# Kernel tuning notes

Hardware: AMD Instinct MI355X
Metric: run time of the kernel (lower is better)

The kernel has to match this reference:

```python
import jax, jax.numpy as jnp
import numpy as np
import math

S = 64.0
M = 0.5
COS_M = math.cos(M)
SIN_M = math.sin(M)
TH = math.cos(math.pi - M)
MM = math.sin(math.pi - M) * M
NUM_CLASSES = 100000
EMB_DIM = 512
BATCH = 512
EPS_CLAMP = 1e-07


def setup_inputs() -> dict:
    key = jax.random.key(0)
    k1, k2, k3 = jax.random.split(key, 3)
    embeddings = jax.random.normal(k1, (BATCH, EMB_DIM), dtype=jnp.float32)
    weight = jax.random.normal(k2, (NUM_CLASSES, EMB_DIM), dtype=jnp.float32)
    labels = jax.random.randint(k3, (BATCH,), 0, NUM_CLASSES, dtype=jnp.int64)
    return {"embeddings": embeddings, "weight": weight, "labels": labels}


def _l2_normalize(x, axis=-1, eps=1e-12):
    # matches F.normalize(p=2): divide by max(norm, eps)
    norm = jnp.sqrt(jnp.sum(x * x, axis=axis, keepdims=True))
    return x / jnp.maximum(norm, eps)


def reference(embeddings, weight, labels):
    e = _l2_normalize(embeddings, axis=1)          # [B, D]
    w = _l2_normalize(weight, axis=1)              # [C, D]
    cosine = jnp.clip(e @ w.T, -1.0 + EPS_CLAMP, 1.0 - EPS_CLAMP)  # [B, C]
    sine = jnp.sqrt(1.0 - cosine * cosine)
    phi = cosine * COS_M - sine * SIN_M
    phi = jnp.where(cosine > TH, phi, cosine - MM)
    one_hot = jax.nn.one_hot(labels, NUM_CLASSES, dtype=cosine.dtype)
    logits = (one_hot * phi + (1.0 - one_hot) * cosine) * S
    # cross-entropy with mean reduction
    logp = jax.nn.log_softmax(logits, axis=-1)
    nll = -jnp.take_along_axis(logp, labels[:, None], axis=1)[:, 0]
    return jnp.mean(nll)
```

## Files before the change

### kernel.cpp

```cpp
#include <hip/hip_runtime.h>
#include <math.h>

#define BATCH 512
#define DIM 512
#define NCLS 100000
#define NB_TILES 391
#define NPART 1564
#define NB_TILES_FB 782
#define S_SCALE 64.0f
#define COS_M 0.8775825618903728f
#define SIN_M 0.479425538604203f
#define TH_C (-0.8775825618903728f)
#define MM_C 0.2397127693021015f
#define CLIP_LO (-1.0f + 1e-7f)
#define CLIP_HI (1.0f - 1e-7f)

typedef __attribute__((ext_vector_type(8))) short bf16x8;
typedef __attribute__((ext_vector_type(4))) float f32x4;

__device__ __forceinline__ unsigned int f2bf(float x) {
    union { float f; unsigned int u; } v;
    v.f = x;
    return (v.u + 0x7fffu + ((v.u >> 16) & 1u)) >> 16;
}
__device__ __forceinline__ unsigned int pack2(float lo, float hi) {
    return f2bf(lo) | (f2bf(hi) << 16);
}

__device__ __forceinline__ void gld_lds16(const void* g, void* l) {
    __builtin_amdgcn_global_load_lds(
        (const __attribute__((address_space(1))) void*)g,
        (__attribute__((address_space(3))) void*)l, 16, 0, 0);
}

__global__ void k_norm_e(const float* __restrict__ e, short* __restrict__ ebf,
                         float* __restrict__ sumexpz) {
    int row = blockIdx.x;
    int tid = threadIdx.x;
    const float4* p = (const float4*)(e + (size_t)row * DIM);
    float4 v = p[tid];
    float ss = v.x * v.x + v.y * v.y + v.z * v.z + v.w * v.w;
    for (int m = 1; m < 64; m <<= 1) ss += __shfl_xor(ss, m, 64);
    __shared__ float wss[2];
    if ((tid & 63) == 0) wss[tid >> 6] = ss;
    __syncthreads();
    float inv = 1.0f / fmaxf(sqrtf(wss[0] + wss[1]), 1e-12f);
    ushort4 o;
    o.x = (unsigned short)f2bf(v.x * inv);
    o.y = (unsigned short)f2bf(v.y * inv);
    o.z = (unsigned short)f2bf(v.z * inv);
    o.w = (unsigned short)f2bf(v.w * inv);
    ((ushort4*)(ebf + (size_t)row * DIM))[tid] = o;
    if (tid == 0) sumexpz[row] = 0.0f;
}

__global__ void k_wconv(const float* __restrict__ w, short* __restrict__ wbf,
                        float* __restrict__ wnorm) {
    int tid = threadIdx.x;
    int wv = tid >> 6, lane = tid & 63;
    int row = blockIdx.x * 4 + wv;
    const float4* src = (const float4*)(w + (size_t)row * DIM);
    float4 a = src[lane];
    float4 b = src[64 + lane];
    float ssq = a.x * a.x + a.y * a.y + a.z * a.z + a.w * a.w +
                b.x * b.x + b.y * b.y + b.z * b.z + b.w * b.w;
#pragma unroll
    for (int m = 1; m < 64; m <<= 1) ssq += __shfl_xor(ssq, m, 64);
    ushort4 oa, ob;
    oa.x = (unsigned short)f2bf(a.x);
    oa.y = (unsigned short)f2bf(a.y);
    oa.z = (unsigned short)f2bf(a.z);
    oa.w = (unsigned short)f2bf(a.w);
    ob.x = (unsigned short)f2bf(b.x);
    ob.y = (unsigned short)f2bf(b.y);
    ob.z = (unsigned short)f2bf(b.z);
    ob.w = (unsigned short)f2bf(b.w);
    ushort4* dst = (ushort4*)(wbf + (size_t)row * DIM);
    dst[lane] = oa;
    dst[64 + lane] = ob;
    if (lane == 0) wnorm[row] = 1.0f / fmaxf(sqrtf(ssq), 1e-12f);
}

__global__ __launch_bounds__(512, 4) void k_gemm2(
    const short* __restrict__ ebf, const short* __restrict__ wbf,
    const float* __restrict__ wnorm, const int* __restrict__ labels,
    float* __restrict__ partial, float* __restrict__ phiS) {
    __shared__ __align__(16) short As[3][4096];
    __shared__ __align__(16) short Bs[3][8192];
    __shared__ int sLbl[128];

    int bx = blockIdx.x;
    int nb = (bx >> 5) * 8 + (bx & 7);
    if (nb >= NB_TILES) return;
    int mb = (bx >> 3) & 3;
    int n0 = nb * 256;

    int tid = threadIdx.x;
    int lane = tid & 63;
    int wv = tid >> 6;
    int wm = wv >> 2, wn = wv & 3;
    int quad = lane >> 4, l16 = lane & 15;

    int g = (lane & 3) ^ (((lane >> 2) ^ (lane >> 4)) & 3);
    int r0 = wv * 16 + (lane >> 2);
    const char* gA = (const char*)ebf + (size_t)(mb * 128 + r0) * (DIM * 2) + g * 16;
    int wr0 = n0 + r0;       if (wr0 > NCLS - 1) wr0 = NCLS - 1;
    int wr1 = n0 + 128 + r0; if (wr1 > NCLS - 1) wr1 = NCLS - 1;
    const char* gB0 = (const char*)wbf + (size_t)wr0 * (DIM * 2) + g * 16;
    const char* gB1 = (const char*)wbf + (size_t)wr1 * (DIM * 2) + g * 16;
    int ldsw = wv * 1024;

#define STAGE(BUF, KC)                                                    \
    do {                                                                  \
        int kb_ = (KC) * 64;                                              \
        gld_lds16(gA + kb_, (char*)&As[BUF][0] + ldsw);                   \
        gld_lds16(gB0 + kb_, (char*)&Bs[BUF][0] + ldsw);                  \
        gld_lds16(gB1 + kb_, (char*)&Bs[BUF][0] + 8192 + ldsw);          \
    } while (0)

    STAGE(0, 0);
    STAGE(1, 1);

    if (tid < 128) sLbl[tid] = labels[mb * 128 + tid];

    f32x4 acc[4][4];
#pragma unroll
    for (int i = 0; i < 4; ++i)
#pragma unroll
        for (int j = 0; j < 4; ++j) acc[i][j] = (f32x4){0.f, 0.f, 0.f, 0.f};

    int go = (quad ^ ((l16 ^ (l16 >> 2)) & 3)) * 8;
    int arowb = (wm * 64 + l16) * 32 + go;
    int browb = (wn * 64 + l16) * 32 + go;

    asm volatile("s_waitcnt vmcnt(3)\n\ts_barrier" ::: "memory");

#pragma unroll
    for (int kc = 0; kc < 16; ++kc) {
        int cur = kc % 3;
        if (kc + 2 < 16) STAGE((kc + 2) % 3, kc + 2);
        {
            bf16x8 af[4], bfr[4];
#pragma unroll
            for (int t = 0; t < 4; ++t)
                af[t] = *(const bf16x8*)&As[cur][arowb + t * 16 * 32];
#pragma unroll
            for (int t = 0; t < 4; ++t)
                bfr[t] = *(const bf16x8*)&Bs[cur][browb + t * 16 * 32];
#pragma unroll
            for (int tm = 0; tm < 4; ++tm)
#pragma unroll
                for (int tn = 0; tn < 4; ++tn)
                    acc[tm][tn] = __builtin_amdgcn_mfma_f32_16x16x32_bf16(
                        af[tm], bfr[tn], acc[tm][tn], 0, 0, 0);
        }
        if (kc < 15) {
            if (kc + 2 < 16)
                asm volatile("s_waitcnt vmcnt(3)\n\ts_barrier" ::: "memory");
            else
                asm volatile("s_waitcnt vmcnt(0)\n\ts_barrier" ::: "memory");
        }
    }
#undef STAGE

    float wscale[4];
#pragma unroll
    for (int tn = 0; tn < 4; ++tn) {
        int col = n0 + wn * 64 + tn * 16 + l16;
        if (col > NCLS - 1) col = NCLS - 1;
        wscale[tn] = wnorm[col];
    }

    float rowsum[16];
#pragma unroll
    for (int i = 0; i < 16; ++i) rowsum[i] = 0.0f;

#pragma unroll
    for (int tm = 0; tm < 4; ++tm) {
#pragma unroll
        for (int r = 0; r < 4; ++r) {
            int m_local = wm * 64 + tm * 16 + quad * 4 + r;
            int lbl = sLbl[m_local];
            float rs = 0.0f;
#pragma unroll
            for (int tn = 0; tn < 4; ++tn) {
                float c = acc[tm][tn][r] * wscale[tn];
                c = fminf(fmaxf(c, CLIP_LO), CLIP_HI);
                int col = n0 + wn * 64 + tn * 16 + l16;
                float t = c;
                if (col == lbl) {
                    float sn = sqrtf(fmaxf(1.0f - c * c, 0.0f));
                    float ph = c * COS_M - sn * SIN_M;
                    ph = (c > TH_C) ? ph : (c - MM_C);
                    t = ph;
                    phiS[mb * 128 + m_local] = S_SCALE * ph;
                }
                float ex = (col < NCLS) ? __expf(S_SCALE * t - 64.0f) : 0.0f;
                rs += ex;
            }
            rowsum[tm * 4 + r] = rs;
        }
    }
    float* pbase = partial + (size_t)(nb * 4 + wn) * 512 + mb * 128;
#pragma unroll
    for (int idx = 0; idx < 16; ++idx) {
        float v = rowsum[idx];
        v += __shfl_xor(v, 1, 64);
        v += __shfl_xor(v, 2, 64);
        v += __shfl_xor(v, 4, 64);
        v += __shfl_xor(v, 8, 64);
        if (l16 == idx) {
            int tm = idx >> 2, r = idx & 3;
            int m_local = wm * 64 + tm * 16 + quad * 4 + r;
            pbase[m_local] = v;
        }
    }
}

__global__ void k_rownll(const float* __restrict__ partial,
                         float* __restrict__ part2) {
    int gid = blockIdx.x * 256 + threadIdx.x;
    int col = ((blockIdx.x & 1) << 8) | threadIdx.x;
    int seg = gid >> 9;
    int p0 = seg * 98;
    int p1 = p0 + 98; if (p1 > NPART) p1 = NPART;
    float s = 0.0f;
#pragma unroll 4
    for (int p = p0; p < p1; ++p) s += partial[(size_t)p * 512 + col];
    part2[seg * 512 + col] = s;
}

__global__ void k_final_mean(const float* __restrict__ part2,
                             const float* __restrict__ phiS,
                             float* __restrict__ out) {
    int tid = threadIdx.x;
    float s = 0.0f;
#pragma unroll
    for (int seg = 0; seg < 16; ++seg) s += part2[seg * 512 + tid];
    float nll = 64.0f + logf(s) - phiS[tid];
    for (int m = 1; m < 64; m <<= 1) nll += __shfl_xor(nll, m, 64);
    __shared__ float ws[8];
    if ((tid & 63) == 0) ws[tid >> 6] = nll;
    __syncthreads();
    if (tid == 0) {
        float t = 0.0f;
        for (int j = 0; j < 8; ++j) t += ws[j];
        out[0] = t / (float)BATCH;
    }
}

__global__ __launch_bounds__(256, 2) void k_gemm_fb(
    const short* __restrict__ ebf, const float* __restrict__ wgt,
    const int* __restrict__ labels, float* __restrict__ sumexp,
    float* __restrict__ phiS) {
    __shared__ __align__(16) short As[128 * 32];
    __shared__ __align__(16) short Bs[128 * 32];
    __shared__ int sLbl[128];
    __shared__ float sWn[128];

    int bx = blockIdx.x;
    int nb = (bx >> 5) * 8 + (bx & 7);
    if (nb >= NB_TILES_FB) return;
    int mb = (bx >> 3) & 3;
    int n0 = nb * 128;

    int tid = threadIdx.x;
    int lane = tid & 63;
    int wv = tid >> 6;
    int wm = wv >> 1, wn = wv & 1;
    int quad = lane >> 4, l16 = lane & 15;

    if (tid < 128) sLbl[tid] = labels[mb * 128 + tid];

    int ar = tid >> 2;
    const short* gA = ebf + (size_t)(mb * 128 + ar) * DIM + (tid & 3) * 8;
    int akey = ((tid >> 2) ^ (tid >> 4)) & 3;
    int aw0 = ar * 32 + ((tid & 3) ^ akey) * 8;

    int br = tid >> 3;
    int gBo[4];
#pragma unroll
    for (int i = 0; i < 4; ++i) {
        int wr = n0 + 32 * i + br;
        if (wr > NCLS - 1) wr = NCLS - 1;
        gBo[i] = wr * DIM + (tid & 7) * 4;
    }
    int bkey = ((tid >> 3) ^ (tid >> 5)) & 3;
    int bw0 = br * 32 + (((tid & 7) >> 1) ^ bkey) * 8 + (tid & 1) * 4;

    f32x4 acc[4][4];
#pragma unroll
    for (int i = 0; i < 4; ++i)
#pragma unroll
        for (int j = 0; j < 4; ++j) acc[i][j] = (f32x4){0.f, 0.f, 0.f, 0.f};
    float ssq[4] = {0.f, 0.f, 0.f, 0.f};

    int go = (quad ^ ((l16 ^ (l16 >> 2)) & 3)) * 8;
    int arowb = (wm * 64 + l16) * 32 + go;
    int browb = (wn * 64 + l16) * 32 + go;

    int4 ra0 = *(const int4*)(gA);
    int4 ra1 = *(const int4*)(gA + 64 * DIM);
    float4 rb0 = *(const float4*)(wgt + gBo[0]);
    float4 rb1 = *(const float4*)(wgt + gBo[1]);
    float4 rb2 = *(const float4*)(wgt + gBo[2]);
    float4 rb3 = *(const float4*)(wgt + gBo[3]);

#pragma unroll 1
    for (int kc = 0; kc < 16; ++kc) {
        *(int4*)&As[aw0] = ra0;
        *(int4*)&As[64 * 32 + aw0] = ra1;
        {
            uint2 p;
            ssq[0] += rb0.x * rb0.x + rb0.y * rb0.y + rb0.z * rb0.z + rb0.w * rb0.w;
            p.x = pack2(rb0.x, rb0.y); p.y = pack2(rb0.z, rb0.w);
            *(uint2*)&Bs[bw0] = p;
            ssq[1] += rb1.x * rb1.x + rb1.y * rb1.y + rb1.z * rb1.z + rb1.w * rb1.w;
            p.x = pack2(rb1.x, rb1.y); p.y = pack2(rb1.z, rb1.w);
            *(uint2*)&Bs[1024 + bw0] = p;
            ssq[2] += rb2.x * rb2.x + rb2.y * rb2.y + rb2.z * rb2.z + rb2.w * rb2.w;
            p.x = pack2(rb2.x, rb2.y); p.y = pack2(rb2.z, rb2.w);
            *(uint2*)&Bs[2048 + bw0] = p;
            ssq[3] += rb3.x * rb3.x + rb3.y * rb3.y + rb3.z * rb3.z + rb3.w * rb3.w;
            p.x = pack2(rb3.x, rb3.y); p.y = pack2(rb3.z, rb3.w);
            *(uint2*)&Bs[3072 + bw0] = p;
        }
        if (kc < 15) {
            int ko = (kc + 1) * 32;
            ra0 = *(const int4*)(gA + ko);
            ra1 = *(const int4*)(gA + 64 * DIM + ko);
            rb0 = *(const float4*)(wgt + gBo[0] + ko);
            rb1 = *(const float4*)(wgt + gBo[1] + ko);
            rb2 = *(const float4*)(wgt + gBo[2] + ko);
            rb3 = *(const float4*)(wgt + gBo[3] + ko);
        }
        asm volatile("s_waitcnt lgkmcnt(0)\n\ts_barrier" ::: "memory");
        {
            bf16x8 af[4], bfr[4];
#pragma unroll
            for (int t = 0; t < 4; ++t)
                af[t] = *(const bf16x8*)&As[arowb + t * 16 * 32];
#pragma unroll
            for (int t = 0; t < 4; ++t)
                bfr[t] = *(const bf16x8*)&Bs[browb + t * 16 * 32];
#pragma unroll
            for (int tm = 0; tm < 4; ++tm)
#pragma unroll
                for (int tn = 0; tn < 4; ++tn)
                    acc[tm][tn] = __builtin_amdgcn_mfma_f32_16x16x32_bf16(
                        af[tm], bfr[tn], acc[tm][tn], 0, 0, 0);
        }
        asm volatile("s_barrier" ::: "memory");
    }

#pragma unroll
    for (int i = 0; i < 4; ++i) {
        float s = ssq[i];
        s += __shfl_xor(s, 1, 64);
        s += __shfl_xor(s, 2, 64);
        s += __shfl_xor(s, 4, 64);
        if ((lane & 7) == 0)
            sWn[32 * i + br] = 1.0f / fmaxf(sqrtf(s), 1e-12f);
    }
    asm volatile("s_waitcnt lgkmcnt(0)\n\ts_barrier" ::: "memory");

    float wscale[4];
#pragma unroll
    for (int tn = 0; tn < 4; ++tn) wscale[tn] = sWn[wn * 64 + tn * 16 + l16];

    float rowsum[16];
#pragma unroll
    for (int i = 0; i < 16; ++i) rowsum[i] = 0.0f;

#pragma unroll
    for (int tm = 0; tm < 4; ++tm) {
#pragma unroll
        for (int r = 0; r < 4; ++r) {
            int m_local = wm * 64 + tm * 16 + quad * 4 + r;
            int lbl = sLbl[m_local];
            float rs = 0.0f;
#pragma unroll
            for (int tn = 0; tn < 4; ++tn) {
                float c = acc[tm][tn][r] * wscale[tn];
                c = fminf(fmaxf(c, CLIP_LO), CLIP_HI);
                int col = n0 + wn * 64 + tn * 16 + l16;
                float t = c;
                if (col == lbl) {
                    float sn = sqrtf(fmaxf(1.0f - c * c, 0.0f));
                    float ph = c * COS_M - sn * SIN_M;
                    ph = (c > TH_C) ? ph : (c - MM_C);
                    t = ph;
                    phiS[mb * 128 + m_local] = S_SCALE * ph;
                }
                float ex = (col < NCLS) ? __expf(S_SCALE * t - 64.0f) : 0.0f;
                rs += ex;
            }
            rowsum[tm * 4 + r] = rs;
        }
    }
#pragma unroll
    for (int idx = 0; idx < 16; ++idx) {
        float v = rowsum[idx];
        v += __shfl_xor(v, 1, 64);
        v += __shfl_xor(v, 2, 64);
        v += __shfl_xor(v, 4, 64);
        v += __shfl_xor(v, 8, 64);
        if (l16 == idx) {
            int tm = idx >> 2, r = idx & 3;
            int m_local = wm * 64 + tm * 16 + quad * 4 + r;
            atomicAdd(&sumexp[mb * 128 + m_local], v);
        }
    }
}

__global__ void k_final_fb(const float* __restrict__ sumexp,
                           const float* __restrict__ phiS,
                           float* __restrict__ out) {
    int tid = threadIdx.x;
    float nll = 64.0f + logf(sumexp[tid]) - phiS[tid];
    for (int m = 1; m < 64; m <<= 1) nll += __shfl_xor(nll, m, 64);
    __shared__ float ws[8];
    if ((tid & 63) == 0) ws[tid >> 6] = nll;
    __syncthreads();
    if (tid == 0) {
        float s = 0.0f;
        for (int j = 0; j < 8; ++j) s += ws[j];
        out[0] = s / (float)BATCH;
    }
}

extern "C" void kernel_launch(void* const* d_in, const int* in_sizes, int n_in,
                              void* d_out, int out_size, void* d_ws,
                              size_t ws_size, hipStream_t stream) {
    const float* emb = (const float*)d_in[0];
    const float* wgt = (const float*)d_in[1];
    const int* lbl = (const int*)d_in[2];

    char* ws = (char*)d_ws;
    short* ebf = (short*)ws;
    float* phiS = (float*)(ws + 524288);
    float* sumexp_fb = (float*)(ws + 526336);
    float* part2 = (float*)(ws + 528384);
    float* wnorm = (float*)(ws + 561152);
    float* partial = (float*)(ws + 1048576);
    short* wbf = (short*)(ws + 4251648);

    const size_t NEED = 4251648ull + 102400000ull;

    if (ws_size >= NEED) {
        k_wconv<<<dim3(NCLS / 4), dim3(256), 0, stream>>>(wgt, wbf, wnorm);
        k_norm_e<<<dim3(BATCH), dim3(128), 0, stream>>>(emb, ebf, sumexp_fb);
        k_gemm2<<<dim3(1568), dim3(512), 0, stream>>>(ebf, wbf, wnorm, lbl,
                                                      partial, phiS);
        k_rownll<<<dim3(32), dim3(256), 0, stream>>>(partial, part2);
        k_final_mean<<<dim3(1), dim3(512), 0, stream>>>(part2, phiS,
                                                        (float*)d_out);
    } else {
        k_norm_e<<<dim3(BATCH), dim3(128), 0, stream>>>(emb, ebf, sumexp_fb);
        k_gemm_fb<<<dim3(3136), dim3(256), 0, stream>>>(ebf, wgt, lbl,
                                                        sumexp_fb, phiS);
        k_final_fb<<<dim3(1), dim3(512), 0, stream>>>(sumexp_fb, phiS,
                                                      (float*)d_out);
    }
}
```

Baseline: 378.4 us.

## Use 4 waves per GEMM block with 64x128 warp tiles

Shrinks the GEMM block from 8 waves to 4 while keeping the 128x256 block tile. Each wave now computes a 64x128 tile with 32 MFMA accumulators and issues six global-to-LDS loads per stage. Partial sums per tile drop from 4 to 2 column groups, so the reduction and workspace layout are resized to match. The goal is more MFMA work per LDS fragment read and fewer partials, at the cost of roughly double the accumulator registers per wave, lower occupancy and fewer waves to hide memory latency.

Result: slower. 390.1 us (+3.1%).

```diff
diff --git a/kernel.cpp b/kernel.cpp
--- a/kernel.cpp
+++ b/kernel.cpp
@@ -5,7 +5,7 @@
 #define DIM 512
 #define NCLS 100000
 #define NB_TILES 391
-#define NPART 1564
+#define NPART 782
 #define NB_TILES_FB 782
 #define S_SCALE 64.0f
 #define COS_M 0.8775825618903728f
@@ -81,7 +81,7 @@
     if (lane == 0) wnorm[row] = 1.0f / fmaxf(sqrtf(ssq), 1e-12f);
 }
 
-__global__ __launch_bounds__(512, 4) void k_gemm2(
+__global__ __launch_bounds__(256, 2) void k_gemm2(
     const short* __restrict__ ebf, const short* __restrict__ wbf,
     const float* __restrict__ wnorm, const int* __restrict__ labels,
     float* __restrict__ partial, float* __restrict__ phiS) {
@@ -98,75 +98,91 @@
     int tid = threadIdx.x;
     int lane = tid & 63;
     int wv = tid >> 6;
-    int wm = wv >> 2, wn = wv & 3;
+    int wm = wv >> 1, wn = wv & 1;
     int quad = lane >> 4, l16 = lane & 15;
 
+    if (tid < 128) sLbl[tid] = labels[mb * 128 + tid];
+
     int g = (lane & 3) ^ (((lane >> 2) ^ (lane >> 4)) & 3);
-    int r0 = wv * 16 + (lane >> 2);
-    const char* gA = (const char*)ebf + (size_t)(mb * 128 + r0) * (DIM * 2) + g * 16;
-    int wr0 = n0 + r0;       if (wr0 > NCLS - 1) wr0 = NCLS - 1;
-    int wr1 = n0 + 128 + r0; if (wr1 > NCLS - 1) wr1 = NCLS - 1;
-    const char* gB0 = (const char*)wbf + (size_t)wr0 * (DIM * 2) + g * 16;
-    const char* gB1 = (const char*)wbf + (size_t)wr1 * (DIM * 2) + g * 16;
-    int ldsw = wv * 1024;
-
-#define STAGE(BUF, KC)                                                    \
-    do {                                                                  \
-        int kb_ = (KC) * 64;                                              \
-        gld_lds16(gA + kb_, (char*)&As[BUF][0] + ldsw);                   \
-        gld_lds16(gB0 + kb_, (char*)&Bs[BUF][0] + ldsw);                  \
-        gld_lds16(gB1 + kb_, (char*)&Bs[BUF][0] + 8192 + ldsw);          \
+    int rr = lane >> 2;
+    const char* gA0 =
+        (const char*)ebf + (size_t)(mb * 128 + wv * 32 + rr) * 1024 + g * 16;
+    const char* gA1 = gA0 + 16 * 1024;
+    const char* gB0;
+    const char* gB1;
+    const char* gB2;
+    const char* gB3;
+    {
+        int w0 = n0 + wv * 64 + rr;       if (w0 > NCLS - 1) w0 = NCLS - 1;
+        int w1 = n0 + wv * 64 + 16 + rr;  if (w1 > NCLS - 1) w1 = NCLS - 1;
+        int w2 = n0 + wv * 64 + 32 + rr;  if (w2 > NCLS - 1) w2 = NCLS - 1;
+        int w3 = n0 + wv * 64 + 48 + rr;  if (w3 > NCLS - 1) w3 = NCLS - 1;
+        gB0 = (const char*)wbf + (size_t)w0 * 1024 + g * 16;
+        gB1 = (const char*)wbf + (size_t)w1 * 1024 + g * 16;
+        gB2 = (const char*)wbf + (size_t)w2 * 1024 + g * 16;
+        gB3 = (const char*)wbf + (size_t)w3 * 1024 + g * 16;
+    }
+    int ldsA = wv * 2048;
+    int ldsB = wv * 4096;
+
+#define STAGE(BUF, KC)                                                   \
+    do {                                                                 \
+        int kb_ = (KC) * 64;                                             \
+        gld_lds16(gA0 + kb_, (char*)&As[BUF][0] + ldsA);                 \
+        gld_lds16(gA1 + kb_, (char*)&As[BUF][0] + ldsA + 1024);          \
+        gld_lds16(gB0 + kb_, (char*)&Bs[BUF][0] + ldsB);                 \
+        gld_lds16(gB1 + kb_, (char*)&Bs[BUF][0] + ldsB + 1024);         \
+        gld_lds16(gB2 + kb_, (char*)&Bs[BUF][0] + ldsB + 2048);         \
+        gld_lds16(gB3 + kb_, (char*)&Bs[BUF][0] + ldsB + 3072);         \
     } while (0)
 
     STAGE(0, 0);
     STAGE(1, 1);
 
-    if (tid < 128) sLbl[tid] = labels[mb * 128 + tid];
-
-    f32x4 acc[4][4];
+    f32x4 acc[4][8];
 #pragma unroll
     for (int i = 0; i < 4; ++i)
 #pragma unroll
-        for (int j = 0; j < 4; ++j) acc[i][j] = (f32x4){0.f, 0.f, 0.f, 0.f};
+        for (int j = 0; j < 8; ++j) acc[i][j] = (f32x4){0.f, 0.f, 0.f, 0.f};
 
     int go = (quad ^ ((l16 ^ (l16 >> 2)) & 3)) * 8;
     int arowb = (wm * 64 + l16) * 32 + go;
-    int browb = (wn * 64 + l16) * 32 + go;
-
-    asm volatile("s_waitcnt vmcnt(3)\n\ts_barrier" ::: "memory");
+    int browb = (wn * 128 + l16) * 32 + go;
+
+    asm volatile("s_waitcnt vmcnt(6)\n\ts_barrier" ::: "memory");
 
 #pragma unroll
     for (int kc = 0; kc < 16; ++kc) {
         int cur = kc % 3;
         if (kc + 2 < 16) STAGE((kc + 2) % 3, kc + 2);
         {
-            bf16x8 af[4], bfr[4];
+            bf16x8 af[4], bfr[8];
 #pragma unroll
             for (int t = 0; t < 4; ++t)
                 af[t] = *(const bf16x8*)&As[cur][arowb + t * 16 * 32];
 #pragma unroll
-            for (int t = 0; t < 4; ++t)
+            for (int t = 0; t < 8; ++t)
                 bfr[t] = *(const bf16x8*)&Bs[cur][browb + t * 16 * 32];
 #pragma unroll
             for (int tm = 0; tm < 4; ++tm)
 #pragma unroll
-                for (int tn = 0; tn < 4; ++tn)
+                for (int tn = 0; tn < 8; ++tn)
                     acc[tm][tn] = __builtin_amdgcn_mfma_f32_16x16x32_bf16(
                         af[tm], bfr[tn], acc[tm][tn], 0, 0, 0);
         }
         if (kc < 15) {
             if (kc + 2 < 16)
-                asm volatile("s_waitcnt vmcnt(3)\n\ts_barrier" ::: "memory");
+                asm volatile("s_waitcnt vmcnt(6)\n\ts_barrier" ::: "memory");
             else
                 asm volatile("s_waitcnt vmcnt(0)\n\ts_barrier" ::: "memory");
         }
     }
 #undef STAGE
 
-    float wscale[4];
-#pragma unroll
-    for (int tn = 0; tn < 4; ++tn) {
-        int col = n0 + wn * 64 + tn * 16 + l16;
+    float wscale[8];
+#pragma unroll
+    for (int tn = 0; tn < 8; ++tn) {
+        int col = n0 + wn * 128 + tn * 16 + l16;
         if (col > NCLS - 1) col = NCLS - 1;
         wscale[tn] = wnorm[col];
     }
@@ -183,10 +199,10 @@
             int lbl = sLbl[m_local];
             float rs = 0.0f;
 #pragma unroll
-            for (int tn = 0; tn < 4; ++tn) {
+            for (int tn = 0; tn < 8; ++tn) {
                 float c = acc[tm][tn][r] * wscale[tn];
                 c = fminf(fmaxf(c, CLIP_LO), CLIP_HI);
-                int col = n0 + wn * 64 + tn * 16 + l16;
+                int col = n0 + wn * 128 + tn * 16 + l16;
                 float t = c;
                 if (col == lbl) {
                     float sn = sqrtf(fmaxf(1.0f - c * c, 0.0f));
@@ -201,7 +217,7 @@
             rowsum[tm * 4 + r] = rs;
         }
     }
-    float* pbase = partial + (size_t)(nb * 4 + wn) * 512 + mb * 128;
+    float* pbase = partial + (size_t)(nb * 2 + wn) * 512 + mb * 128;
 #pragma unroll
     for (int idx = 0; idx < 16; ++idx) {
         float v = rowsum[idx];
@@ -222,8 +238,8 @@
     int gid = blockIdx.x * 256 + threadIdx.x;
     int col = ((blockIdx.x & 1) << 8) | threadIdx.x;
     int seg = gid >> 9;
-    int p0 = seg * 98;
-    int p1 = p0 + 98; if (p1 > NPART) p1 = NPART;
+    int p0 = seg * 49;
+    int p1 = p0 + 49; if (p1 > NPART) p1 = NPART;
     float s = 0.0f;
 #pragma unroll 4
     for (int p = p0; p < p1; ++p) s += partial[(size_t)p * 512 + col];
@@ -443,14 +459,14 @@
     float* part2 = (float*)(ws + 528384);
     float* wnorm = (float*)(ws + 561152);
     float* partial = (float*)(ws + 1048576);
-    short* wbf = (short*)(ws + 4251648);
-
-    const size_t NEED = 4251648ull + 102400000ull;
+    short* wbf = (short*)(ws + 2650112);
+
+    const size_t NEED = 2650112ull + 102400000ull;
 
     if (ws_size >= NEED) {
         k_wconv<<<dim3(NCLS / 4), dim3(256), 0, stream>>>(wgt, wbf, wnorm);
         k_norm_e<<<dim3(BATCH), dim3(128), 0, stream>>>(emb, ebf, sumexp_fb);
-        k_gemm2<<<dim3(1568), dim3(512), 0, stream>>>(ebf, wbf, wnorm, lbl,
+        k_gemm2<<<dim3(1568), dim3(256), 0, stream>>>(ebf, wbf, wnorm, lbl,
                                                       partial, phiS);
         k_rownll<<<dim3(32), dim3(256), 0, stream>>>(partial, part2);
         k_final_mean<<<dim3(1), dim3(512), 0, stream>>>(part2, phiS,
```

## Fuse weight bf16 conversion and norm computation into GEMM, retile to 256x128

Applied to the files above, without the earlier changes.

Removes the separate weight-conversion kernel that wrote a bf16 copy of the 100000x512 weight matrix plus per-row inverse norms. The GEMM now loads fp32 weights directly through registers, accumulates per-row sum of squares, packs to bf16 into LDS, and computes the inverse norms in shared memory. Tiles are reshaped so each block covers 256 batch rows by 128 classes, meaning each weight row is read once per block pair instead of four times. This avoids a full write and reread of the bf16 weight matrix, at the cost of register-staged B loads, lower occupancy, and twice the fp32 weight reads.

After: 404.4 us. 6.9% more time.

```diff
diff --git a/kernel.cpp b/kernel.cpp
--- a/kernel.cpp
+++ b/kernel.cpp
@@ -4,7 +4,7 @@
 #define BATCH 512
 #define DIM 512
 #define NCLS 100000
-#define NB_TILES 391
+#define NB_TILES 782
 #define NPART 1564
 #define NB_TILES_FB 782
 #define S_SCALE 64.0f
@@ -54,91 +54,98 @@
     if (tid == 0) sumexpz[row] = 0.0f;
 }
 
-__global__ void k_wconv(const float* __restrict__ w, short* __restrict__ wbf,
-                        float* __restrict__ wnorm) {
-    int tid = threadIdx.x;
-    int wv = tid >> 6, lane = tid & 63;
-    int row = blockIdx.x * 4 + wv;
-    const float4* src = (const float4*)(w + (size_t)row * DIM);
-    float4 a = src[lane];
-    float4 b = src[64 + lane];
-    float ssq = a.x * a.x + a.y * a.y + a.z * a.z + a.w * a.w +
-                b.x * b.x + b.y * b.y + b.z * b.z + b.w * b.w;
-#pragma unroll
-    for (int m = 1; m < 64; m <<= 1) ssq += __shfl_xor(ssq, m, 64);
-    ushort4 oa, ob;
-    oa.x = (unsigned short)f2bf(a.x);
-    oa.y = (unsigned short)f2bf(a.y);
-    oa.z = (unsigned short)f2bf(a.z);
-    oa.w = (unsigned short)f2bf(a.w);
-    ob.x = (unsigned short)f2bf(b.x);
-    ob.y = (unsigned short)f2bf(b.y);
-    ob.z = (unsigned short)f2bf(b.z);
-    ob.w = (unsigned short)f2bf(b.w);
-    ushort4* dst = (ushort4*)(wbf + (size_t)row * DIM);
-    dst[lane] = oa;
-    dst[64 + lane] = ob;
-    if (lane == 0) wnorm[row] = 1.0f / fmaxf(sqrtf(ssq), 1e-12f);
-}
-
-__global__ __launch_bounds__(512, 4) void k_gemm2(
-    const short* __restrict__ ebf, const short* __restrict__ wbf,
-    const float* __restrict__ wnorm, const int* __restrict__ labels,
-    float* __restrict__ partial, float* __restrict__ phiS) {
-    __shared__ __align__(16) short As[3][4096];
-    __shared__ __align__(16) short Bs[3][8192];
-    __shared__ int sLbl[128];
+__global__ __launch_bounds__(512, 2) void k_gemm3(
+    const short* __restrict__ ebf, const float* __restrict__ wgt,
+    const int* __restrict__ labels, float* __restrict__ partial,
+    float* __restrict__ phiS) {
+    __shared__ __align__(16) short As[3][8192];
+    __shared__ __align__(16) short Bs[3][4096];
+    __shared__ int sLbl[256];
+    __shared__ float sWn[128];
 
     int bx = blockIdx.x;
-    int nb = (bx >> 5) * 8 + (bx & 7);
+    int nb = (bx >> 4) * 8 + (bx & 7);
     if (nb >= NB_TILES) return;
-    int mb = (bx >> 3) & 3;
-    int n0 = nb * 256;
+    int mb = (bx >> 3) & 1;
+    int n0 = nb * 128;
 
     int tid = threadIdx.x;
     int lane = tid & 63;
     int wv = tid >> 6;
-    int wm = wv >> 2, wn = wv & 3;
+    int wm = wv >> 1, wn = wv & 1;
     int quad = lane >> 4, l16 = lane & 15;
 
+    if (tid < 256) sLbl[tid] = labels[mb * 256 + tid];
+
     int g = (lane & 3) ^ (((lane >> 2) ^ (lane >> 4)) & 3);
-    int r0 = wv * 16 + (lane >> 2);
-    const char* gA = (const char*)ebf + (size_t)(mb * 128 + r0) * (DIM * 2) + g * 16;
-    int wr0 = n0 + r0;       if (wr0 > NCLS - 1) wr0 = NCLS - 1;
-    int wr1 = n0 + 128 + r0; if (wr1 > NCLS - 1) wr1 = NCLS - 1;
-    const char* gB0 = (const char*)wbf + (size_t)wr0 * (DIM * 2) + g * 16;
-    const char* gB1 = (const char*)wbf + (size_t)wr1 * (DIM * 2) + g * 16;
-    int ldsw = wv * 1024;
-
-#define STAGE(BUF, KC)                                                    \
-    do {                                                                  \
-        int kb_ = (KC) * 64;                                              \
-        gld_lds16(gA + kb_, (char*)&As[BUF][0] + ldsw);                   \
-        gld_lds16(gB0 + kb_, (char*)&Bs[BUF][0] + ldsw);                  \
-        gld_lds16(gB1 + kb_, (char*)&Bs[BUF][0] + 8192 + ldsw);          \
+    const char* gA0 = (const char*)ebf +
+                      (size_t)(mb * 256 + wv * 32 + (lane >> 2)) * 1024 + g * 16;
+    const char* gA1 = gA0 + 16 * 1024;
+    int ldsA = wv * 2048;
+
+    int brow = tid >> 2;
+    int wr = n0 + brow;
+    if (wr > NCLS - 1) wr = NCLS - 1;
+    const float* gB = wgt + (size_t)wr * DIM + (tid & 3) * 8;
+    int bkey = (brow ^ (brow >> 2)) & 3;
+    int bw0 = brow * 32 + ((tid & 3) ^ bkey) * 8;
+
+#define STAGE_A(BUF, KC)                                        \
+    do {                                                        \
+        int kb_ = (KC) * 64;                                    \
+        gld_lds16(gA0 + kb_, (char*)&As[BUF][0] + ldsA);        \
+        gld_lds16(gA1 + kb_, (char*)&As[BUF][0] + ldsA + 1024); \
     } while (0)
 
-    STAGE(0, 0);
-    STAGE(1, 1);
-
-    if (tid < 128) sLbl[tid] = labels[mb * 128 + tid];
+#define LOAD_B(R0, R1, KC)                         \
+    do {                                           \
+        R0 = *(const float4*)(gB + (KC) * 32);     \
+        R1 = *(const float4*)(gB + (KC) * 32 + 4); \
+    } while (0)
+
+#define WRITE_B(BUF, R0, R1)                                               \
+    do {                                                                   \
+        ssq += R0.x * R0.x + R0.y * R0.y + R0.z * R0.z + R0.w * R0.w +     \
+               R1.x * R1.x + R1.y * R1.y + R1.z * R1.z + R1.w * R1.w;      \
+        int4 pv;                                                           \
+        pv.x = (int)pack2(R0.x, R0.y);                                     \
+        pv.y = (int)pack2(R0.z, R0.w);                                     \
+        pv.z = (int)pack2(R1.x, R1.y);                                     \
+        pv.w = (int)pack2(R1.z, R1.w);                                     \
+        *(int4*)&Bs[BUF][bw0] = pv;                                        \
+    } while (0)
 
     f32x4 acc[4][4];
 #pragma unroll
     for (int i = 0; i < 4; ++i)
 #pragma unroll
         for (int j = 0; j < 4; ++j) acc[i][j] = (f32x4){0.f, 0.f, 0.f, 0.f};
+    float ssq = 0.0f;
 
     int go = (quad ^ ((l16 ^ (l16 >> 2)) & 3)) * 8;
     int arowb = (wm * 64 + l16) * 32 + go;
     int browb = (wn * 64 + l16) * 32 + go;
 
-    asm volatile("s_waitcnt vmcnt(3)\n\ts_barrier" ::: "memory");
+    float4 e0, e1, o0, o1;
+    LOAD_B(e0, e1, 0);
+    STAGE_A(0, 0);
+    STAGE_A(1, 1);
+    WRITE_B(0, e0, e1);
+    LOAD_B(o0, o1, 1);
+    asm volatile("s_waitcnt vmcnt(4) lgkmcnt(0)\n\ts_barrier" ::: "memory");
 
 #pragma unroll
     for (int kc = 0; kc < 16; ++kc) {
         int cur = kc % 3;
-        if (kc + 2 < 16) STAGE((kc + 2) % 3, kc + 2);
+        if (kc + 2 < 16) {
+            STAGE_A((kc + 2) % 3, kc + 2);
+            if (kc & 1) LOAD_B(o0, o1, kc + 2);
+            else        LOAD_B(e0, e1, kc + 2);
+        }
+        if (kc < 15) {
+            if (kc & 1) WRITE_B((kc + 1) % 3, e0, e1);
+            else        WRITE_B((kc + 1) % 3, o0, o1);
+        }
         {
             bf16x8 af[4], bfr[4];
 #pragma unroll
@@ -154,22 +161,24 @@
                     acc[tm][tn] = __builtin_amdgcn_mfma_f32_16x16x32_bf16(
                         af[tm], bfr[tn], acc[tm][tn], 0, 0, 0);
         }
-        if (kc < 15) {
-            if (kc + 2 < 16)
-                asm volatile("s_waitcnt vmcnt(3)\n\ts_barrier" ::: "memory");
-            else
-                asm volatile("s_waitcnt vmcnt(0)\n\ts_barrier" ::: "memory");
-        }
-    }
-#undef STAGE
+        if (kc < 15)
+            asm volatile("s_waitcnt lgkmcnt(0)\n\ts_barrier" ::: "memory");
+    }
+#undef STAGE_A
+#undef LOAD_B
+#undef WRITE_B
+
+    {
+        float s = ssq;
+        s += __shfl_xor(s, 1, 64);
+        s += __shfl_xor(s, 2, 64);
+        if ((tid & 3) == 0) sWn[brow] = 1.0f / fmaxf(sqrtf(s), 1e-12f);
+    }
+    asm volatile("s_waitcnt lgkmcnt(0)\n\ts_barrier" ::: "memory");
 
     float wscale[4];
 #pragma unroll
-    for (int tn = 0; tn < 4; ++tn) {
-        int col = n0 + wn * 64 + tn * 16 + l16;
-        if (col > NCLS - 1) col = NCLS - 1;
-        wscale[tn] = wnorm[col];
-    }
+    for (int tn = 0; tn < 4; ++tn) wscale[tn] = sWn[wn * 64 + tn * 16 + l16];
 
     float rowsum[16];
 #pragma unroll
@@ -193,7 +202,7 @@
                     float ph = c * COS_M - sn * SIN_M;
                     ph = (c > TH_C) ? ph : (c - MM_C);
                     t = ph;
-                    phiS[mb * 128 + m_local] = S_SCALE * ph;
+                    phiS[mb * 256 + m_local] = S_SCALE * ph;
                 }
                 float ex = (col < NCLS) ? __expf(S_SCALE * t - 64.0f) : 0.0f;
                 rs += ex;
@@ -201,7 +210,7 @@
             rowsum[tm * 4 + r] = rs;
         }
     }
-    float* pbase = partial + (size_t)(nb * 4 + wn) * 512 + mb * 128;
+    float* pbase = partial + (size_t)(nb * 2 + wn) * 512 + mb * 256;
 #pragma unroll
     for (int idx = 0; idx < 16; ++idx) {
         float v = rowsum[idx];
@@ -441,17 +450,14 @@
     float* phiS = (float*)(ws + 524288);
     float* sumexp_fb = (float*)(ws + 526336);
     float* part2 = (float*)(ws + 528384);
-    float* wnorm = (float*)(ws + 561152);
     float* partial = (float*)(ws + 1048576);
-    short* wbf = (short*)(ws + 4251648);
-
-    const size_t NEED = 4251648ull + 102400000ull;
+
+    const size_t NEED = 4251648ull;
 
     if (ws_size >= NEED) {
-        k_wconv<<<dim3(NCLS / 4), dim3(256), 0, stream>>>(wgt, wbf, wnorm);
         k_norm_e<<<dim3(BATCH), dim3(128), 0, stream>>>(emb, ebf, sumexp_fb);
-        k_gemm2<<<dim3(1568), dim3(512), 0, stream>>>(ebf, wbf, wnorm, lbl,
-                                                      partial, phiS);
+        k_gemm3<<<dim3(1568), dim3(512), 0, stream>>>(ebf, wgt, lbl, partial,
+                                                      phiS);
         k_rownll<<<dim3(32), dim3(256), 0, stream>>>(partial, part2);
         k_final_mean<<<dim3(1), dim3(512), 0, stream>>>(part2, phiS,
                                                         (float*)d_out);
```
